# Optimization experiments

Hardware: AMD Instinct MI355X
Metric: run time of the kernel (lower is better)

Reference implementation:

```python
import jax, jax.numpy as jnp
import numpy as np

HEADS = 8
NUM_LANDMARKS = 256
PINV_ITERS = 6
KERNEL = 33
PAD = KERNEL // 2


def moore_penrose_iter_pinv(x, iters=PINV_ITERS):
    abs_x = jnp.abs(x)
    col = abs_x.sum(axis=-1)
    row = abs_x.sum(axis=-2)
    z = jnp.swapaxes(x, -1, -2) / (jnp.max(col) * jnp.max(row))
    I = jnp.eye(x.shape[-1], dtype=x.dtype)
    for _ in range(iters):
        xz = x @ z
        z = 0.25 * z @ (13.0 * I - xz @ (15.0 * I - xz @ (7.0 * I - xz)))
    return z


def setup_inputs() -> dict:
    key = jax.random.key(0)
    k1, k2, k3, k4 = jax.random.split(key, 4)
    b, h, n, d = 2, HEADS, 8192, 64
    q = jax.random.normal(k1, (b, h, n, d), dtype=jnp.float32)
    k = jax.random.normal(k2, (b, h, n, d), dtype=jnp.float32)
    v = jax.random.normal(k3, (b, h, n, d), dtype=jnp.float32)
    conv_w = jax.random.normal(k4, (HEADS, 1, KERNEL, 1), dtype=jnp.float32) * 0.05
    return {"q": q, "k": k, "v": v, "conv_w": conv_w}


def reference(q, k, v, conv_w):
    b, h, n, d = q.shape
    m = NUM_LANDMARKS
    l = n // m  # n chosen divisible by m, so no padding branch

    # landmarks: mean over contiguous groups of size l
    q_land = q.reshape(b, h, m, l, d).sum(axis=-2) / l  # [b,h,m,d]
    k_land = k.reshape(b, h, m, l, d).sum(axis=-2) / l

    sim1 = jnp.einsum('bhid,bhjd->bhij', q, k_land)       # [b,h,n,m]
    sim2 = jnp.einsum('bhid,bhjd->bhij', q_land, k_land)  # [b,h,m,m]
    sim3 = jnp.einsum('bhid,bhjd->bhij', q_land, k)       # [b,h,m,n]

    attn1 = jax.nn.softmax(sim1, axis=-1)
    attn2 = jax.nn.softmax(sim2, axis=-1)
    attn3 = jax.nn.softmax(sim3, axis=-1)

    attn2_inv = moore_penrose_iter_pinv(attn2, PINV_ITERS)

    out = attn1 @ (attn2_inv @ (attn3 @ v))  # [b,h,n,d]

    # depthwise residual conv over sequence dim (Conv2d(h,h,(33,1),groups=h,bias=False) on v)
    res = jax.lax.conv_general_dilated(
        v, conv_w,
        window_strides=(1, 1),
        padding=((PAD, PAD), (0, 0)),
        dimension_numbers=('NCHW', 'OIHW', 'NCHW'),
        feature_group_count=HEADS,
    )
    return out + res
```

## Files before the change

### kernel.cpp

```cpp
#include <hip/hip_runtime.h>


#define N_SEQ 8192
#define NBH   16
#define MLAND 256
#define DHEAD 64
#define NSPLIT3 8
#define MM_E  (NBH * MLAND * MLAND)
#define LM_E  (NBH * MLAND * DHEAD)

typedef __attribute__((ext_vector_type(8))) short bfrag;
typedef __attribute__((ext_vector_type(8))) _Float16 hfrag;
typedef __attribute__((ext_vector_type(4))) float f32x4;

__device__ __forceinline__ void fma8(float (&o)[8], float p, const float4& a, const float4& b) {
    o[0] += p * a.x; o[1] += p * a.y; o[2] += p * a.z; o[3] += p * a.w;
    o[4] += p * b.x; o[5] += p * b.y; o[6] += p * b.z; o[7] += p * b.w;
}

__device__ __forceinline__ float bf2f(unsigned short h) {
    return __uint_as_float(((unsigned)h) << 16);
}

__device__ __forceinline__ void splitbf(float v, unsigned short& h, unsigned short& l) {
    unsigned bits = __float_as_uint(v);
    h = (unsigned short)(bits >> 16);
    float r = v - __uint_as_float(bits & 0xffff0000u);
    l = (unsigned short)(__float_as_uint(r) >> 16);
}

__device__ __forceinline__ void splith(float v, unsigned short& h, unsigned short& l) {
    _Float16 hf = (_Float16)v;
    _Float16 lf = (_Float16)(v - (float)hf);
    h = __builtin_bit_cast(unsigned short, hf);
    l = __builtin_bit_cast(unsigned short, lf);
}

__device__ __forceinline__ void stage16(const float* __restrict__ src,
                                        unsigned short* dh, unsigned short* dl) {
    unsigned* ph = (unsigned*)dh;
    unsigned* pl = (unsigned*)dl;
    #pragma unroll
    for (int o = 0; o < 16; o += 4) {
        float4 a = *(const float4*)(src + o);
        float vv[4] = {a.x, a.y, a.z, a.w};
        unsigned short h[4], l[4];
        #pragma unroll
        for (int u = 0; u < 4; ++u) splitbf(vv[u], h[u], l[u]);
        ph[o / 2]     = (unsigned)h[0] | ((unsigned)h[1] << 16);
        ph[o / 2 + 1] = (unsigned)h[2] | ((unsigned)h[3] << 16);
        pl[o / 2]     = (unsigned)l[0] | ((unsigned)l[1] << 16);
        pl[o / 2 + 1] = (unsigned)l[2] | ((unsigned)l[3] << 16);
    }
}

__device__ __forceinline__ void stageh16(const float* __restrict__ src,
                                         unsigned short* dh, unsigned short* dl) {
    unsigned* ph = (unsigned*)dh;
    unsigned* pl = (unsigned*)dl;
    #pragma unroll
    for (int o = 0; o < 16; o += 4) {
        float4 a = *(const float4*)(src + o);
        float vv[4] = {a.x, a.y, a.z, a.w};
        unsigned short h[4], l[4];
        #pragma unroll
        for (int u = 0; u < 4; ++u) splith(vv[u], h[u], l[u]);
        ph[o / 2]     = (unsigned)h[0] | ((unsigned)h[1] << 16);
        ph[o / 2 + 1] = (unsigned)h[2] | ((unsigned)h[3] << 16);
        pl[o / 2]     = (unsigned)l[0] | ((unsigned)l[1] << 16);
        pl[o / 2 + 1] = (unsigned)l[2] | ((unsigned)l[3] << 16);
    }
}

__global__ __launch_bounds__(64) void k_landmarks(
    const float* __restrict__ q, const float* __restrict__ k,
    float* __restrict__ ql, float* __restrict__ kl)
{
    int mi = blockIdx.x & 255;
    int bh = blockIdx.x >> 8;
    const float* src = blockIdx.y ? k : q;
    float*       dst = blockIdx.y ? kl : ql;
    int t = threadIdx.x;
    const float* s = src + ((size_t)bh * N_SEQ + (size_t)mi * 32) * DHEAD;
    float acc = 0.f;
    #pragma unroll
    for (int j = 0; j < 32; ++j) acc += s[j * DHEAD + t];
    dst[((size_t)bh * MLAND + mi) * DHEAD + t] = acc * (1.f / 32.f);
}

__global__ __launch_bounds__(256) void k_sim2_softmax(
    const float* __restrict__ ql, const float* __restrict__ kl,
    unsigned short* __restrict__ xs)
{
    unsigned short* xh = xs;
    unsigned short* xl = xs + MM_E;
    int bh = blockIdx.x >> 8;
    int i  = blockIdx.x & 255;
    int t  = threadIdx.x;
    __shared__ float qrow[DHEAD];
    __shared__ float wred[8];
    if (t < DHEAD) qrow[t] = ql[((size_t)bh * MLAND + i) * DHEAD + t];
    __syncthreads();
    const float* krow = kl + ((size_t)bh * MLAND + t) * DHEAD;
    float s = 0.f;
    #pragma unroll
    for (int kk = 0; kk < DHEAD; kk += 4) {
        float4 k4 = *(const float4*)(krow + kk);
        s += qrow[kk] * k4.x + qrow[kk + 1] * k4.y + qrow[kk + 2] * k4.z + qrow[kk + 3] * k4.w;
    }
    float m = s;
    #pragma unroll
    for (int o = 32; o > 0; o >>= 1) m = fmaxf(m, __shfl_xor(m, o, 64));
    int wave = t >> 6, lane = t & 63;
    if (lane == 0) wred[wave] = m;
    __syncthreads();
    float bm = fmaxf(fmaxf(wred[0], wred[1]), fmaxf(wred[2], wred[3]));
    float e = __expf(s - bm);
    float sum = e;
    #pragma unroll
    for (int o = 32; o > 0; o >>= 1) sum += __shfl_xor(sum, o, 64);
    if (lane == 0) wred[4 + wave] = sum;
    __syncthreads();
    float bs = wred[4] + wred[5] + wred[6] + wred[7];
    float val = e / bs;
    unsigned short h, l;
    splitbf(val, h, l);
    size_t idx = ((size_t)bh * MLAND + i) * MLAND + t;
    xh[idx] = h;
    xl[idx] = l;
}

__global__ __launch_bounds__(256) void k_scale_reduce(
    const unsigned short* __restrict__ xs, float* __restrict__ scl)
{
    const unsigned short* xh = xs;
    const unsigned short* xl = xs + MM_E;
    int bh = blockIdx.x, t = threadIdx.x;
    size_t b = (size_t)bh * MLAND * MLAND;
    float colsum = 0.f, rowsum = 0.f;
    for (int i = 0; i < MLAND; ++i) {
        size_t idx = b + (size_t)i * MLAND + t;
        colsum += bf2f(xh[idx]) + bf2f(xl[idx]);
    }
    for (int j = 0; j < MLAND; ++j) {
        size_t idx = b + (size_t)t * MLAND + j;
        rowsum += bf2f(xh[idx]) + bf2f(xl[idx]);
    }
    __shared__ float red[256];
    red[t] = rowsum;
    __syncthreads();
    for (int o = 128; o > 0; o >>= 1) {
        if (t < o) red[t] = fmaxf(red[t], red[t + o]);
        __syncthreads();
    }
    if (t == 0) atomicMax((unsigned int*)&scl[0], __float_as_uint(red[0]));
    __syncthreads();
    red[t] = colsum;
    __syncthreads();
    for (int o = 128; o > 0; o >>= 1) {
        if (t < o) red[t] = fmaxf(red[t], red[t + o]);
        __syncthreads();
    }
    if (t == 0) atomicMax((unsigned int*)&scl[1], __float_as_uint(red[0]));
}

__global__ __launch_bounds__(256) void k_zinit(
    const unsigned short* __restrict__ xs, unsigned short* __restrict__ zs,
    const float* __restrict__ scl)
{
    const unsigned short* xh = xs;
    const unsigned short* xl = xs + MM_E;
    unsigned short* zh = zs;
    unsigned short* zl = zs + MM_E;
    __shared__ float tile[32][33];
    int bh = blockIdx.z;
    int i0 = blockIdx.y * 32, j0 = blockIdx.x * 32;
    int t = threadIdx.x;
    int lx = t & 31, ly = t >> 5;
    size_t b = (size_t)bh * MLAND * MLAND;
    #pragma unroll
    for (int p = 0; p < 4; ++p) {
        size_t idx = b + (size_t)(i0 + ly + 8 * p) * MLAND + j0 + lx;
        tile[ly + 8 * p][lx] = bf2f(xh[idx]) + bf2f(xl[idx]);
    }
    __syncthreads();
    float inv = 1.0f / (scl[0] * scl[1]);
    #pragma unroll
    for (int p = 0; p < 4; ++p) {
        float val = tile[lx][ly + 8 * p] * inv;
        unsigned short h, l;
        splitbf(val, h, l);
        size_t idx = b + (size_t)(j0 + ly + 8 * p) * MLAND + i0 + lx;
        zh[idx] = h;
        zl[idx] = l;
    }
}

__global__ __launch_bounds__(256) void k_bmm_planes(
    const unsigned short* __restrict__ Ahp, const unsigned short* __restrict__ Alp,
    const unsigned short* __restrict__ Bhp, const unsigned short* __restrict__ Blp,
    unsigned short* __restrict__ Chp, unsigned short* __restrict__ Clp,
    float* __restrict__ Cf,
    int N, float diag, float bscale, float outscale)
{
    __shared__ unsigned short sm[4 * 64 * 72];
    unsigned short* Ah = sm;
    unsigned short* Al = sm + 64 * 72;
    unsigned short* Bh = sm + 2 * 64 * 72;
    unsigned short* Bl = sm + 3 * 64 * 72;

    int bh = blockIdx.z;
    const size_t abase = (size_t)bh * 65536;
    const size_t bbase = (size_t)bh * 256 * N;
    int m0 = blockIdx.y * 64, n0 = blockIdx.x * 64;
    int t = threadIdx.x;
    int wave = t >> 6, lane = t & 63;
    int l15 = lane & 15, quad = lane >> 4;
    unsigned sflip = (bscale < 0.f) ? 0x8000u : 0u;

    f32x4 acc[4] = {};

    for (int kc = 0; kc < 256; kc += 64) {
        __syncthreads();
        {
            int m = t & 63, ks = (t >> 6) * 16;
            size_t off = abase + (size_t)(m0 + m) * 256 + kc + ks;
            *(uint4*)&Ah[m * 72 + ks]     = *(const uint4*)&Ahp[off];
            *(uint4*)&Ah[m * 72 + ks + 8] = *(const uint4*)&Ahp[off + 8];
            *(uint4*)&Al[m * 72 + ks]     = *(const uint4*)&Alp[off];
            *(uint4*)&Al[m * 72 + ks + 8] = *(const uint4*)&Alp[off + 8];
        }
        {
            int kk = t & 63, ns = (t >> 6) * 16;
            int gk = kc + kk;
            size_t off = bbase + (size_t)gk * N + n0 + ns;
            unsigned short hb[16], lb[16];
            *(uint4*)&hb[0] = *(const uint4*)&Bhp[off];
            *(uint4*)&hb[8] = *(const uint4*)&Bhp[off + 8];
            *(uint4*)&lb[0] = *(const uint4*)&Blp[off];
            *(uint4*)&lb[8] = *(const uint4*)&Blp[off + 8];
            #pragma unroll
            for (int u = 0; u < 16; ++u) {
                unsigned short h = hb[u] ^ sflip;
                unsigned short l = lb[u] ^ sflip;
                if (diag != 0.f && gk == n0 + ns + u) {
                    float val = diag + bf2f(h) + bf2f(l);
                    splitbf(val, h, l);
                }
                Bh[(ns + u) * 72 + kk] = h;
                Bl[(ns + u) * 72 + kk] = l;
            }
        }
        __syncthreads();

        #pragma unroll
        for (int k0 = 0; k0 < 64; k0 += 32) {
            int kf = k0 + quad * 8;
            int am = wave * 16 + l15;
            bfrag ah = *(const bfrag*)&Ah[am * 72 + kf];
            bfrag al = *(const bfrag*)&Al[am * 72 + kf];
            #pragma unroll
            for (int j = 0; j < 4; ++j) {
                int bn = j * 16 + l15;
                bfrag bhf = *(const bfrag*)&Bh[bn * 72 + kf];
                bfrag blf = *(const bfrag*)&Bl[bn * 72 + kf];
                acc[j] = __builtin_amdgcn_mfma_f32_16x16x32_bf16(al, bhf, acc[j], 0, 0, 0);
                acc[j] = __builtin_amdgcn_mfma_f32_16x16x32_bf16(ah, blf, acc[j], 0, 0, 0);
                acc[j] = __builtin_amdgcn_mfma_f32_16x16x32_bf16(ah, bhf, acc[j], 0, 0, 0);
            }
        }
    }

    size_t cbase = (size_t)bh * 256 * N;
    if (Cf) {
        #pragma unroll
        for (int j = 0; j < 4; ++j) {
            #pragma unroll
            for (int r = 0; r < 4; ++r) {
                int row = m0 + wave * 16 + quad * 4 + r;
                Cf[cbase + (size_t)row * N + n0 + j * 16 + l15] = acc[j][r] * outscale;
            }
        }
    } else {
        #pragma unroll
        for (int j = 0; j < 4; ++j) {
            #pragma unroll
            for (int r = 0; r < 4; ++r) {
                int row = m0 + wave * 16 + quad * 4 + r;
                float val = acc[j][r] * outscale;
                unsigned short h, l;
                splitbf(val, h, l);
                size_t idx = cbase + (size_t)row * N + n0 + j * 16 + l15;
                Chp[idx] = h;
                Clp[idx] = l;
            }
        }
    }
}

__global__ __launch_bounds__(256, 2) void k_attn3_partial(
    const float* __restrict__ ql, const float* __restrict__ k,
    const float* __restrict__ v, float* __restrict__ pO,
    float* __restrict__ pm, float* __restrict__ pl)
{
    __shared__ __align__(16) unsigned short sm3[36864];
    unsigned short* QH = sm3;
    unsigned short* QL = sm3 + 4608;
    unsigned short* KH = sm3 + 9216;
    unsigned short* KL = sm3 + 13824;
    unsigned short* VH = sm3 + 18432;
    unsigned short* VL = sm3 + 23040;
    unsigned short* PH = sm3 + 27648;
    unsigned short* PL = sm3 + 32256;

    int sp = blockIdx.x;
    int m0 = blockIdx.y * 64;
    int bh = blockIdx.z;
    int t = threadIdx.x;
    int wave = t >> 6, lane = t & 63;
    int l15 = lane & 15, quad = lane >> 4;

    {
        int row = t & 63, ds = (t >> 6) * 16;
        const float* src = ql + ((size_t)bh * MLAND + m0 + row) * DHEAD + ds;
        stage16(src, &QH[row * 72 + ds], &QL[row * 72 + ds]);
    }
    __syncthreads();

    bfrag aqh[2], aql[2];
    #pragma unroll
    for (int ks = 0; ks < 2; ++ks) {
        aqh[ks] = *(const bfrag*)&QH[(wave * 16 + l15) * 72 + ks * 32 + quad * 8];
        aql[ks] = *(const bfrag*)&QL[(wave * 16 + l15) * 72 + ks * 32 + quad * 8];
    }

    f32x4 O[4] = {};
    float M[4], L[4];
    #pragma unroll
    for (int r = 0; r < 4; ++r) { M[r] = -1e30f; L[r] = 0.f; }

    const float* kb = k + (size_t)bh * N_SEQ * DHEAD;
    const float* vb = v + (size_t)bh * N_SEQ * DHEAD;

    for (int cc = 0; cc < 16; ++cc) {
        int c0 = sp * 1024 + cc * 64;
        __syncthreads();
        {
            int key = t & 63, ds = (t >> 6) * 16;
            stage16(kb + (size_t)(c0 + key) * DHEAD + ds,
                    &KH[key * 72 + ds], &KL[key * 72 + ds]);
        }
        {
            int key = t & 63, dq = (t >> 6) * 16;
            const float* src = vb + (size_t)(c0 + key) * DHEAD + dq;
            #pragma unroll
            for (int o = 0; o < 16; o += 4) {
                float4 a = *(const float4*)(src + o);
                float vv[4] = {a.x, a.y, a.z, a.w};
                #pragma unroll
                for (int u = 0; u < 4; ++u) {
                    unsigned short h, l;
                    splitbf(vv[u], h, l);
                    VH[(dq + o + u) * 72 + key] = h;
                    VL[(dq + o + u) * 72 + key] = l;
                }
            }
        }
        __syncthreads();

        f32x4 S4[4] = {};
        __builtin_amdgcn_s_setprio(1);
        #pragma unroll
        for (int ks = 0; ks < 2; ++ks) {
            #pragma unroll
            for (int ni = 0; ni < 4; ++ni) {
                bfrag bkh = *(const bfrag*)&KH[(ni * 16 + l15) * 72 + ks * 32 + quad * 8];
                bfrag bkl = *(const bfrag*)&KL[(ni * 16 + l15) * 72 + ks * 32 + quad * 8];
                S4[ni] = __builtin_amdgcn_mfma_f32_16x16x32_bf16(aql[ks], bkh, S4[ni], 0, 0, 0);
                S4[ni] = __builtin_amdgcn_mfma_f32_16x16x32_bf16(aqh[ks], bkl, S4[ni], 0, 0, 0);
                S4[ni] = __builtin_amdgcn_mfma_f32_16x16x32_bf16(aqh[ks], bkh, S4[ni], 0, 0, 0);
            }
        }
        __builtin_amdgcn_s_setprio(0);

        #pragma unroll
        for (int r = 0; r < 4; ++r) {
            float mv = fmaxf(fmaxf(S4[0][r], S4[1][r]), fmaxf(S4[2][r], S4[3][r]));
            mv = fmaxf(mv, __shfl_xor(mv, 1, 16));
            mv = fmaxf(mv, __shfl_xor(mv, 2, 16));
            mv = fmaxf(mv, __shfl_xor(mv, 4, 16));
            mv = fmaxf(mv, __shfl_xor(mv, 8, 16));
            float nM = fmaxf(M[r], mv);
            float alpha = __expf(M[r] - nM);
            M[r] = nM;
            float rs = 0.f;
            #pragma unroll
            for (int ni = 0; ni < 4; ++ni) {
                float p = __expf(S4[ni][r] - nM);
                S4[ni][r] = p;
                rs += p;
            }
            rs += __shfl_xor(rs, 1, 16);
            rs += __shfl_xor(rs, 2, 16);
            rs += __shfl_xor(rs, 4, 16);
            rs += __shfl_xor(rs, 8, 16);
            L[r] = L[r] * alpha + rs;
            #pragma unroll
            for (int ni = 0; ni < 4; ++ni) O[ni][r] *= alpha;
        }

        #pragma unroll
        for (int ni = 0; ni < 4; ++ni) {
            #pragma unroll
            for (int r = 0; r < 4; ++r) {
                int row = wave * 16 + quad * 4 + r;
                int col = ni * 16 + l15;
                unsigned short h, l;
                splitbf(S4[ni][r], h, l);
                PH[row * 72 + col] = h;
                PL[row * 72 + col] = l;
            }
        }

        __builtin_amdgcn_s_setprio(1);
        #pragma unroll
        for (int ks = 0; ks < 2; ++ks) {
            bfrag aph = *(const bfrag*)&PH[(wave * 16 + l15) * 72 + ks * 32 + quad * 8];
            bfrag apl = *(const bfrag*)&PL[(wave * 16 + l15) * 72 + ks * 32 + quad * 8];
            #pragma unroll
            for (int ni = 0; ni < 4; ++ni) {
                bfrag bvh = *(const bfrag*)&VH[(ni * 16 + l15) * 72 + ks * 32 + quad * 8];
                bfrag bvl = *(const bfrag*)&VL[(ni * 16 + l15) * 72 + ks * 32 + quad * 8];
                O[ni] = __builtin_amdgcn_mfma_f32_16x16x32_bf16(apl, bvh, O[ni], 0, 0, 0);
                O[ni] = __builtin_amdgcn_mfma_f32_16x16x32_bf16(aph, bvl, O[ni], 0, 0, 0);
                O[ni] = __builtin_amdgcn_mfma_f32_16x16x32_bf16(aph, bvh, O[ni], 0, 0, 0);
            }
        }
        __builtin_amdgcn_s_setprio(0);
    }

    int base = (bh * NSPLIT3 + sp) * MLAND + m0;
    #pragma unroll
    for (int r = 0; r < 4; ++r) {
        int row = wave * 16 + quad * 4 + r;
        if (l15 == 0) { pm[base + row] = M[r]; pl[base + row] = L[r]; }
        #pragma unroll
        for (int ni = 0; ni < 4; ++ni)
            pO[(size_t)(base + row) * DHEAD + ni * 16 + l15] = O[ni][r];
    }
}

__global__ __launch_bounds__(64) void k_attn3_combine(
    const float* __restrict__ pO, const float* __restrict__ pm,
    const float* __restrict__ pl, unsigned short* __restrict__ kvs)
{
    unsigned short* kvh = kvs;
    unsigned short* kvl = kvs + LM_E;
    int bh = blockIdx.x >> 8;
    int m  = blockIdx.x & 255;
    int d  = threadIdx.x;
    float M = -1e30f;
    #pragma unroll
    for (int s = 0; s < NSPLIT3; ++s) M = fmaxf(M, pm[(bh * NSPLIT3 + s) * MLAND + m]);
    float L = 0.f, O = 0.f;
    #pragma unroll
    for (int s = 0; s < NSPLIT3; ++s) {
        int base = (bh * NSPLIT3 + s) * MLAND + m;
        float w = __expf(pm[base] - M);
        L += pl[base] * w;
        O += w * pO[(size_t)base * DHEAD + d];
    }
    float val = O / L;
    unsigned short h, l;
    splitbf(val, h, l);
    size_t idx = ((size_t)bh * MLAND + m) * DHEAD + d;
    kvh[idx] = h;
    kvl[idx] = l;
}

__global__ __launch_bounds__(256, 2) void k_attn1_mfma(
    const float* __restrict__ q, const float* __restrict__ kl,
    const float* __restrict__ W, float* __restrict__ out)
{
    __shared__ __align__(16) unsigned short sm1[36864];
    unsigned short* QH = sm1;
    unsigned short* QL = sm1 + 4608;
    unsigned short* KH = sm1 + 9216;
    unsigned short* KL = sm1 + 13824;
    unsigned short* WH = sm1 + 18432;
    unsigned short* WL = sm1 + 23040;
    unsigned short* PH = sm1 + 27648;
    unsigned short* PL = sm1 + 32256;

    int bh = blockIdx.y;
    int r0 = blockIdx.x * 64;
    int t = threadIdx.x;
    int wave = t >> 6, lane = t & 63;
    int l15 = lane & 15, quad = lane >> 4;

    {
        int row = t & 63, ds = (t >> 6) * 16;
        const float* src = q + ((size_t)bh * N_SEQ + r0 + row) * DHEAD + ds;
        stageh16(src, &QH[row * 72 + ds], &QL[row * 72 + ds]);
    }
    __syncthreads();

    hfrag aqh[2], aql[2];
    #pragma unroll
    for (int ks = 0; ks < 2; ++ks) {
        aqh[ks] = *(const hfrag*)&QH[(wave * 16 + l15) * 72 + ks * 32 + quad * 8];
        aql[ks] = *(const hfrag*)&QL[(wave * 16 + l15) * 72 + ks * 32 + quad * 8];
    }

    f32x4 O4[4] = {};
    float M[4], L[4];
    #pragma unroll
    for (int r = 0; r < 4; ++r) { M[r] = -1e30f; L[r] = 0.f; }

    for (int mc = 0; mc < 4; ++mc) {
        __syncthreads();
        {
            int key = t & 63, ds = (t >> 6) * 16;
            stageh16(kl + ((size_t)bh * MLAND + mc * 64 + key) * DHEAD + ds,
                     &KH[key * 72 + ds], &KL[key * 72 + ds]);
        }
        {
            int key = t & 63, dq = (t >> 6) * 16;
            const float* src = W + ((size_t)bh * MLAND + mc * 64 + key) * DHEAD + dq;
            #pragma unroll
            for (int o = 0; o < 16; o += 4) {
                float4 a = *(const float4*)(src + o);
                float vv[4] = {a.x * 0.015625f, a.y * 0.015625f,
                               a.z * 0.015625f, a.w * 0.015625f};
                #pragma unroll
                for (int u = 0; u < 4; ++u) {
                    unsigned short h, l;
                    splith(vv[u], h, l);
                    WH[(dq + o + u) * 72 + key] = h;
                    WL[(dq + o + u) * 72 + key] = l;
                }
            }
        }
        __syncthreads();

        f32x4 S4[4] = {};
        __builtin_amdgcn_s_setprio(1);
        #pragma unroll
        for (int ks = 0; ks < 2; ++ks) {
            #pragma unroll
            for (int ni = 0; ni < 4; ++ni) {
                hfrag bkh = *(const hfrag*)&KH[(ni * 16 + l15) * 72 + ks * 32 + quad * 8];
                hfrag bkl = *(const hfrag*)&KL[(ni * 16 + l15) * 72 + ks * 32 + quad * 8];
                S4[ni] = __builtin_amdgcn_mfma_f32_16x16x32_f16(aql[ks], bkh, S4[ni], 0, 0, 0);
                S4[ni] = __builtin_amdgcn_mfma_f32_16x16x32_f16(aqh[ks], bkl, S4[ni], 0, 0, 0);
                S4[ni] = __builtin_amdgcn_mfma_f32_16x16x32_f16(aqh[ks], bkh, S4[ni], 0, 0, 0);
            }
        }
        __builtin_amdgcn_s_setprio(0);

        #pragma unroll
        for (int r = 0; r < 4; ++r) {
            float mv = fmaxf(fmaxf(S4[0][r], S4[1][r]), fmaxf(S4[2][r], S4[3][r]));
            mv = fmaxf(mv, __shfl_xor(mv, 1, 16));
            mv = fmaxf(mv, __shfl_xor(mv, 2, 16));
            mv = fmaxf(mv, __shfl_xor(mv, 4, 16));
            mv = fmaxf(mv, __shfl_xor(mv, 8, 16));
            float nM = fmaxf(M[r], mv);
            float alpha = __expf(M[r] - nM);
            M[r] = nM;
            float rs = 0.f;
            #pragma unroll
            for (int ni = 0; ni < 4; ++ni) {
                float p = __expf(S4[ni][r] - nM);
                S4[ni][r] = p;
                rs += p;
            }
            rs += __shfl_xor(rs, 1, 16);
            rs += __shfl_xor(rs, 2, 16);
            rs += __shfl_xor(rs, 4, 16);
            rs += __shfl_xor(rs, 8, 16);
            L[r] = L[r] * alpha + rs;
            #pragma unroll
            for (int ni = 0; ni < 4; ++ni) O4[ni][r] *= alpha;
        }

        #pragma unroll
        for (int ni = 0; ni < 4; ++ni) {
            #pragma unroll
            for (int r = 0; r < 4; ++r) {
                int row = wave * 16 + quad * 4 + r;
                int col = ni * 16 + l15;
                unsigned short h, l;
                splith(S4[ni][r], h, l);
                PH[row * 72 + col] = h;
                PL[row * 72 + col] = l;
            }
        }

        __builtin_amdgcn_s_setprio(1);
        #pragma unroll
        for (int ks = 0; ks < 2; ++ks) {
            hfrag aph = *(const hfrag*)&PH[(wave * 16 + l15) * 72 + ks * 32 + quad * 8];
            hfrag apl = *(const hfrag*)&PL[(wave * 16 + l15) * 72 + ks * 32 + quad * 8];
            #pragma unroll
            for (int ni = 0; ni < 4; ++ni) {
                hfrag bwh = *(const hfrag*)&WH[(ni * 16 + l15) * 72 + ks * 32 + quad * 8];
                hfrag bwl = *(const hfrag*)&WL[(ni * 16 + l15) * 72 + ks * 32 + quad * 8];
                O4[ni] = __builtin_amdgcn_mfma_f32_16x16x32_f16(apl, bwh, O4[ni], 0, 0, 0);
                O4[ni] = __builtin_amdgcn_mfma_f32_16x16x32_f16(aph, bwl, O4[ni], 0, 0, 0);
                O4[ni] = __builtin_amdgcn_mfma_f32_16x16x32_f16(aph, bwh, O4[ni], 0, 0, 0);
            }
        }
        __builtin_amdgcn_s_setprio(0);
    }

    float inv[4];
    #pragma unroll
    for (int r = 0; r < 4; ++r) inv[r] = 64.0f / L[r];
    #pragma unroll
    for (int r = 0; r < 4; ++r) {
        int row = wave * 16 + quad * 4 + r;
        float* dst = out + ((size_t)bh * N_SEQ + r0 + row) * DHEAD;
        #pragma unroll
        for (int ni = 0; ni < 4; ++ni)
            dst[ni * 16 + l15] = O4[ni][r] * inv[r];
    }
}

__global__ __launch_bounds__(256) void k_conv_add(
    const float* __restrict__ v, const float* __restrict__ cw,
    float* __restrict__ out)
{
    __shared__ __align__(16) float smem[160 * 68];
    __shared__ float wgt[33];
    int bh = blockIdx.y;
    int r0 = blockIdx.x * 128;
    int t = threadIdx.x;
    int wave = t >> 6, lane = t & 63;
    int ly = lane >> 3, lx = lane & 7;
    int rb = wave * 32 + ly * 4;

    if (t < 33) wgt[t] = cw[(bh & 7) * 33 + t];

    for (int rr = t; rr < 160; rr += 256) {
        int gr = r0 - 16 + rr;
        bool ok = (gr >= 0) && (gr < N_SEQ);
        const float* src = v + ((size_t)bh * N_SEQ + gr) * DHEAD;
        #pragma unroll
        for (int c = 0; c < 64; c += 4) {
            float4 val = ok ? *(const float4*)(src + c) : make_float4(0.f, 0.f, 0.f, 0.f);
            *(float4*)&smem[rr * 68 + c] = val;
        }
    }
    __syncthreads();

    float res[4][8] = {};
    #pragma unroll
    for (int w = 0; w < 36; ++w) {
        float4 va  = *(const float4*)&smem[(rb + w) * 68 + lx * 8];
        float4 vb4 = *(const float4*)&smem[(rb + w) * 68 + lx * 8 + 4];
        #pragma unroll
        for (int i = 0; i < 4; ++i) {
            if (w - i >= 0 && w - i <= 32) {
                float wv = wgt[w - i];
                fma8(res[i], wv, va, vb4);
            }
        }
    }

    #pragma unroll
    for (int i = 0; i < 4; ++i) {
        float* dst = out + ((size_t)bh * N_SEQ + r0 + rb + i) * DHEAD + lx * 8;
        float4 o0 = *(const float4*)dst;
        float4 o1 = *(const float4*)(dst + 4);
        *(float4*)dst = make_float4(o0.x + res[i][0], o0.y + res[i][1],
                                    o0.z + res[i][2], o0.w + res[i][3]);
        *(float4*)(dst + 4) = make_float4(o1.x + res[i][4], o1.y + res[i][5],
                                          o1.z + res[i][6], o1.w + res[i][7]);
    }
}

extern "C" void kernel_launch(void* const* d_in, const int* in_sizes, int n_in,
                              void* d_out, int out_size, void* d_ws, size_t ws_size,
                              hipStream_t stream)
{
    (void)in_sizes; (void)n_in; (void)out_size; (void)ws_size;
    const float* q  = (const float*)d_in[0];
    const float* k  = (const float*)d_in[1];
    const float* v  = (const float*)d_in[2];
    const float* cw = (const float*)d_in[3];
    float* out = (float*)d_out;
    float* ws  = (float*)d_ws;

    const size_t LM = (size_t)LM_E;
    const size_t MM = (size_t)MM_E;

    float* ql  = ws;
    float* kl  = ql  + LM;
    float* xsf = kl  + LM;
    float* zsf = xsf + MM;
    float* big = zsf + MM;
    float* kvf = big + 4 * MM;
    float* W   = kvf + LM;
    float* scl = W   + LM;
    float* pm  = scl + 16;
    float* pl  = pm + (size_t)NBH * NSPLIT3 * MLAND;

    float* pO = big;

    unsigned short* xs  = (unsigned short*)xsf;
    unsigned short* zs  = (unsigned short*)zsf;
    unsigned short* bgu = (unsigned short*)big;
    unsigned short* kvs = (unsigned short*)kvf;

    unsigned short* zh  = zs;
    unsigned short* zl  = zs + MM;
    unsigned short* xh  = xs;
    unsigned short* xl  = xs + MM;
    unsigned short* z2h = bgu;
    unsigned short* z2l = bgu + MM;
    unsigned short* xzh = bgu + 2 * MM;
    unsigned short* xzl = bgu + 3 * MM;
    unsigned short* t2h = bgu + 4 * MM;
    unsigned short* t2l = bgu + 5 * MM;
    unsigned short* t3h = bgu + 6 * MM;
    unsigned short* t3l = bgu + 7 * MM;
    unsigned short* kvh = kvs;
    unsigned short* kvl = kvs + LM;

    hipMemsetAsync(scl, 0, 32, stream);

    k_landmarks<<<dim3(NBH * MLAND, 2), 64, 0, stream>>>(q, k, ql, kl);
    k_sim2_softmax<<<NBH * MLAND, 256, 0, stream>>>(ql, kl, xs);
    k_scale_reduce<<<NBH, 256, 0, stream>>>(xs, scl);
    k_zinit<<<dim3(8, 8, NBH), 256, 0, stream>>>(xs, zs, scl);

    k_attn3_partial<<<dim3(NSPLIT3, 4, NBH), 256, 0, stream>>>(ql, k, v, pO, pm, pl);
    k_attn3_combine<<<NBH * MLAND, 64, 0, stream>>>(pO, pm, pl, kvs);

    unsigned short *zch = zh, *zcl = zl, *znh = z2h, *znl = z2l;
    for (int it = 0; it < 6; ++it) {
        k_bmm_planes<<<dim3(4, 4, NBH), 256, 0, stream>>>(
            xh, xl, zch, zcl, xzh, xzl, nullptr, 256, 0.f, 1.f, 1.f);
        k_bmm_planes<<<dim3(4, 4, NBH), 256, 0, stream>>>(
            xzh, xzl, xzh, xzl, t2h, t2l, nullptr, 256, 7.f, -1.f, 1.f);
        k_bmm_planes<<<dim3(4, 4, NBH), 256, 0, stream>>>(
            xzh, xzl, t2h, t2l, t3h, t3l, nullptr, 256, 15.f, -1.f, 1.f);
        k_bmm_planes<<<dim3(4, 4, NBH), 256, 0, stream>>>(
            zch, zcl, t3h, t3l, znh, znl, nullptr, 256, 13.f, -1.f, 0.25f);
        unsigned short* th = zch; zch = znh; znh = th;
        unsigned short* tl = zcl; zcl = znl; znl = tl;
    }
    k_bmm_planes<<<dim3(1, 4, NBH), 256, 0, stream>>>(
        zch, zcl, kvh, kvl, nullptr, nullptr, W, 64, 0.f, 1.f, 1.f);

    k_attn1_mfma<<<dim3(128, NBH), 256, 0, stream>>>(q, kl, W, out);
    k_conv_add<<<dim3(64, NBH), 256, 0, stream>>>(v, cw, out);
}
```

Baseline: 632.6 us.

## Fuse pinv iteration chain into one cooperative kernel with grid syncs

Replaces 25 separate bmm launches for the Newton-Schulz pseudo-inverse iterations with a single cooperative kernel of 256 blocks. The blocks step through the same tiled matmuls and are separated by grid-wide barriers. The goal is to remove per-launch overhead and the gaps between the many small dependent launches. In exchange, each stage now waits on a grid.sync barrier. The kernel also depends on all 256 blocks fitting at once for the cooperative launch to run.

Measured after the change: 2.057 ms. 225% more time.

```diff
diff --git a/kernel.cpp b/kernel.cpp
--- a/kernel.cpp
+++ b/kernel.cpp
@@ -1,4 +1,7 @@
 #include <hip/hip_runtime.h>
+#include <hip/hip_cooperative_groups.h>
+
+namespace cg = cooperative_groups;
 
 
 #define N_SEQ 8192
@@ -196,27 +199,23 @@
     }
 }
 
-__global__ __launch_bounds__(256) void k_bmm_planes(
-    const unsigned short* __restrict__ Ahp, const unsigned short* __restrict__ Alp,
-    const unsigned short* __restrict__ Bhp, const unsigned short* __restrict__ Blp,
-    unsigned short* __restrict__ Chp, unsigned short* __restrict__ Clp,
-    float* __restrict__ Cf,
-    int N, float diag, float bscale, float outscale)
-{
-    __shared__ unsigned short sm[4 * 64 * 72];
+__device__ __forceinline__ void bmm_tile(
+    unsigned short* sm,
+    const unsigned short* Ahp, const unsigned short* Alp,
+    const unsigned short* Bhp, const unsigned short* Blp,
+    unsigned short* Chp, unsigned short* Clp, float* Cf,
+    int N, float diag, unsigned sflip, float outscale,
+    int bh, int m0, int n0, int t)
+{
     unsigned short* Ah = sm;
     unsigned short* Al = sm + 64 * 72;
     unsigned short* Bh = sm + 2 * 64 * 72;
     unsigned short* Bl = sm + 3 * 64 * 72;
 
-    int bh = blockIdx.z;
     const size_t abase = (size_t)bh * 65536;
     const size_t bbase = (size_t)bh * 256 * N;
-    int m0 = blockIdx.y * 64, n0 = blockIdx.x * 64;
-    int t = threadIdx.x;
     int wave = t >> 6, lane = t & 63;
     int l15 = lane & 15, quad = lane >> 4;
-    unsigned sflip = (bscale < 0.f) ? 0x8000u : 0u;
 
     f32x4 acc[4] = {};
 
@@ -296,6 +295,43 @@
             }
         }
     }
+}
+
+__global__ __launch_bounds__(256) void k_pinv_chain(
+    const unsigned short* xh, const unsigned short* xl,
+    unsigned short* zh, unsigned short* zl,
+    unsigned short* z2h, unsigned short* z2l,
+    unsigned short* xzh, unsigned short* xzl,
+    unsigned short* t2h, unsigned short* t2l,
+    unsigned short* t3h, unsigned short* t3l,
+    const unsigned short* kvh, const unsigned short* kvl,
+    float* W)
+{
+    cg::grid_group grid = cg::this_grid();
+    __shared__ __align__(16) unsigned short sm[4 * 64 * 72];
+
+    int blk = blockIdx.x;
+    int bh = blk >> 4;
+    int tile = blk & 15;
+    int m0 = (tile >> 2) * 64, n0 = (tile & 3) * 64;
+    int t = threadIdx.x;
+
+    unsigned short *zch = zh, *zcl = zl, *znh = z2h, *znl = z2l;
+
+    for (int it = 0; it < 6; ++it) {
+        bmm_tile(sm, xh, xl, zch, zcl, xzh, xzl, nullptr, 256, 0.f, 0u, 1.f, bh, m0, n0, t);
+        __threadfence(); grid.sync();
+        bmm_tile(sm, xzh, xzl, xzh, xzl, t2h, t2l, nullptr, 256, 7.f, 0x8000u, 1.f, bh, m0, n0, t);
+        __threadfence(); grid.sync();
+        bmm_tile(sm, xzh, xzl, t2h, t2l, t3h, t3l, nullptr, 256, 15.f, 0x8000u, 1.f, bh, m0, n0, t);
+        __threadfence(); grid.sync();
+        bmm_tile(sm, zch, zcl, t3h, t3l, znh, znl, nullptr, 256, 13.f, 0x8000u, 0.25f, bh, m0, n0, t);
+        __threadfence(); grid.sync();
+        unsigned short* th = zch; zch = znh; znh = th;
+        unsigned short* tl = zcl; zcl = znl; znl = tl;
+    }
+    if (n0 == 0)
+        bmm_tile(sm, zch, zcl, kvh, kvl, nullptr, nullptr, W, 64, 0.f, 0u, 1.f, bh, m0, 0, t);
 }
 
 __global__ __launch_bounds__(256, 2) void k_attn3_partial(
@@ -713,10 +749,10 @@
     unsigned short* bgu = (unsigned short*)big;
     unsigned short* kvs = (unsigned short*)kvf;
 
+    unsigned short* xh  = xs;
+    unsigned short* xl  = xs + MM;
     unsigned short* zh  = zs;
     unsigned short* zl  = zs + MM;
-    unsigned short* xh  = xs;
-    unsigned short* xl  = xs + MM;
     unsigned short* z2h = bgu;
     unsigned short* z2l = bgu + MM;
     unsigned short* xzh = bgu + 2 * MM;
@@ -738,21 +774,20 @@
     k_attn3_partial<<<dim3(NSPLIT3, 4, NBH), 256, 0, stream>>>(ql, k, v, pO, pm, pl);
     k_attn3_combine<<<NBH * MLAND, 64, 0, stream>>>(pO, pm, pl, kvs);
 
-    unsigned short *zch = zh, *zcl = zl, *znh = z2h, *znl = z2l;
-    for (int it = 0; it < 6; ++it) {
-        k_bmm_planes<<<dim3(4, 4, NBH), 256, 0, stream>>>(
-            xh, xl, zch, zcl, xzh, xzl, nullptr, 256, 0.f, 1.f, 1.f);
-        k_bmm_planes<<<dim3(4, 4, NBH), 256, 0, stream>>>(
-            xzh, xzl, xzh, xzl, t2h, t2l, nullptr, 256, 7.f, -1.f, 1.f);
-        k_bmm_planes<<<dim3(4, 4, NBH), 256, 0, stream>>>(
-            xzh, xzl, t2h, t2l, t3h, t3l, nullptr, 256, 15.f, -1.f, 1.f);
-        k_bmm_planes<<<dim3(4, 4, NBH), 256, 0, stream>>>(
-            zch, zcl, t3h, t3l, znh, znl, nullptr, 256, 13.f, -1.f, 0.25f);
-        unsigned short* th = zch; zch = znh; znh = th;
-        unsigned short* tl = zcl; zcl = znl; znl = tl;
-    }
-    k_bmm_planes<<<dim3(1, 4, NBH), 256, 0, stream>>>(
-        zch, zcl, kvh, kvl, nullptr, nullptr, W, 64, 0.f, 1.f, 1.f);
+    {
+        void* args[] = {
+            (void*)&xh, (void*)&xl,
+            (void*)&zh, (void*)&zl,
+            (void*)&z2h, (void*)&z2l,
+            (void*)&xzh, (void*)&xzl,
+            (void*)&t2h, (void*)&t2l,
+            (void*)&t3h, (void*)&t3l,
+            (void*)&kvh, (void*)&kvl,
+            (void*)&W
+        };
+        hipLaunchCooperativeKernel((const void*)k_pinv_chain,
+                                   dim3(256), dim3(256), args, 0, stream);
+    }
 
     k_attn1_mfma<<<dim3(128, NBH), 256, 0, stream>>>(q, kl, W, out);
     k_conv_add<<<dim3(64, NBH), 256, 0, stream>>>(v, cw, out);
```
